# Performance work log

Hardware: AMD Instinct MI355X
Metric: run time of the kernel (lower is better)

The kernel has to match this reference:

```python
import jax, jax.numpy as jnp
import numpy as np

N = 8192   # nodes
F = 128    # input feature dim
U = 128    # units
EDGE_P = 0.002  # ~16 avg degree before symmetrization


def setup_inputs() -> dict:
    key = jax.random.key(0)
    k1, k2, k3 = jax.random.split(key, 3)
    a = (jax.random.uniform(k1, (N, N)) < EDGE_P).astype(jnp.float32)
    adj = jnp.maximum(a, a.T)  # symmetric binary adjacency, no self-loops
    x = jax.random.normal(k2, (N, F), dtype=jnp.float32)
    W = jax.random.normal(k3, (F, U), dtype=jnp.float32) * 0.05
    b = jnp.zeros((U,), dtype=jnp.float32)
    return {"x": x, "adj": adj, "W": W, "b": b}


def adj_norm(adj):
    # Kipf & Welling renormalization: A' = D^{-1/2} (A + I) D^{-1/2}
    a_hat = adj + jnp.eye(adj.shape[0], dtype=adj.dtype)
    d_inv_sqrt = jax.lax.rsqrt(jnp.sum(a_hat, axis=-1))
    return a_hat * d_inv_sqrt[:, None] * d_inv_sqrt[None, :]


def reference(x, adj, W, b):
    adj_n = adj_norm(adj)            # [N, N]
    h = adj_n @ x                    # [N, F] aggregation
    h = h @ W + b                    # [N, U] dense projection + bias
    return jax.nn.relu(h)
```

## Files before the change

### kernel.cpp

```cpp
#include <hip/hip_runtime.h>
#include <math.h>

#define N 8192
#define F 128
#define U 128
#define CAP 128
#define GEMM_BLOCKS 256
#define FCHUNK 32

typedef float f32x4 __attribute__((ext_vector_type(4)));
typedef unsigned short u16;
typedef unsigned int u32;

__device__ __forceinline__ int lane_off(unsigned long long m) {
    int c = __builtin_amdgcn_mbcnt_lo((unsigned)m, 0u);
    return __builtin_amdgcn_mbcnt_hi((unsigned)(m >> 32), c);
}

__device__ __forceinline__ u16 f2bf(float f) {
    u32 u = __float_as_uint(f);
    return (u16)((u + 0x7fffu + ((u >> 16) & 1u)) >> 16);
}
__device__ __forceinline__ float bflo(u32 v) { return __uint_as_float(v << 16); }
__device__ __forceinline__ float bfhi(u32 v) { return __uint_as_float(v & 0xffff0000u); }

__global__ __launch_bounds__(256) void k_scan_gemm(const float* __restrict__ adj,
                                                   const float* __restrict__ x,
                                                   const float* __restrict__ W,
                                                   float* __restrict__ dinv,
                                                   int* __restrict__ cnt,
                                                   u16* __restrict__ cols,
                                                   u16* __restrict__ y) {
    __shared__ float sW[FCHUNK * U];
    const int tid = threadIdx.x;

    if (blockIdx.x < GEMM_BLOCKS) {
        const int l  = tid & 31;
        const int p  = tid >> 5;
        const int n0 = blockIdx.x * 32 + p * 4;
        const float* xr = x + (size_t)n0 * F;

        float acc[4][4];
        #pragma unroll
        for (int i = 0; i < 4; ++i)
            #pragma unroll
            for (int u = 0; u < 4; ++u) acc[i][u] = 0.f;

        for (int chunk = 0; chunk < F / FCHUNK; ++chunk) {
            {
                const float4* Wp = (const float4*)(W + (size_t)chunk * FCHUNK * U);
                float4* sWp = (float4*)sW;
                #pragma unroll
                for (int k = 0; k < (FCHUNK * U / 4) / 256; ++k)
                    sWp[tid + k * 256] = Wp[tid + k * 256];
            }
            __syncthreads();

            const int fb = chunk * FCHUNK;
            #pragma unroll
            for (int f = 0; f < FCHUNK; f += 4) {
                f32x4 xa = *(const f32x4*)(xr + 0 * F + fb + f);
                f32x4 xb = *(const f32x4*)(xr + 1 * F + fb + f);
                f32x4 xc = *(const f32x4*)(xr + 2 * F + fb + f);
                f32x4 xd = *(const f32x4*)(xr + 3 * F + fb + f);
                #pragma unroll
                for (int k = 0; k < 4; ++k) {
                    const f32x4 w = *(const f32x4*)(sW + (f + k) * U + l * 4);
                    #pragma unroll
                    for (int u = 0; u < 4; ++u) {
                        acc[0][u] = fmaf(xa[k], w[u], acc[0][u]);
                        acc[1][u] = fmaf(xb[k], w[u], acc[1][u]);
                        acc[2][u] = fmaf(xc[k], w[u], acc[2][u]);
                        acc[3][u] = fmaf(xd[k], w[u], acc[3][u]);
                    }
                }
            }
            __syncthreads();
        }

        #pragma unroll
        for (int i = 0; i < 4; ++i) {
            ushort4 o;
            o.x = f2bf(acc[i][0]);
            o.y = f2bf(acc[i][1]);
            o.z = f2bf(acc[i][2]);
            o.w = f2bf(acc[i][3]);
            *(ushort4*)(y + (size_t)(n0 + i) * U + l * 4) = o;
        }
    } else {
        const int wid  = tid >> 6;
        const int lane = tid & 63;
        const int row  = (blockIdx.x - GEMM_BLOCKS) * 4 + wid;

        const f32x4* rp = (const f32x4*)(adj + (size_t)row * N);
        u16* crow = cols + (size_t)row * CAP;

        int base = 0;

        #pragma unroll 8
        for (int k = 0; k < N / 4 / 64; ++k) {
            const int fi = k * 64 + lane;
            const f32x4 v = __builtin_nontemporal_load(&rp[fi]);
            const int col = fi * 4;

            const unsigned long long m0 = __ballot(v[0] != 0.f);
            const unsigned long long m1 = __ballot(v[1] != 0.f);
            const unsigned long long m2 = __ballot(v[2] != 0.f);
            const unsigned long long m3 = __ballot(v[3] != 0.f);

            if (m0) { if (v[0] != 0.f) { int s = base + lane_off(m0); if (s < CAP) crow[s] = (u16)col;       } base += __popcll(m0); }
            if (m1) { if (v[1] != 0.f) { int s = base + lane_off(m1); if (s < CAP) crow[s] = (u16)(col + 1); } base += __popcll(m1); }
            if (m2) { if (v[2] != 0.f) { int s = base + lane_off(m2); if (s < CAP) crow[s] = (u16)(col + 2); } base += __popcll(m2); }
            if (m3) { if (v[3] != 0.f) { int s = base + lane_off(m3); if (s < CAP) crow[s] = (u16)(col + 3); } base += __popcll(m3); }
        }

        if (lane == 0) {
            dinv[row] = 1.0f / sqrtf((float)base + 1.0f);
            cnt[row]  = min(base, CAP);
        }
    }
}

__global__ __launch_bounds__(256, 4) void k_agg(const u16* __restrict__ y,
                                                const float* __restrict__ bias,
                                                const float* __restrict__ dinv,
                                                const int* __restrict__ cnt,
                                                const u16* __restrict__ cols,
                                                float* __restrict__ out) {
    const int wid  = threadIdx.x >> 6;
    const int lane = threadIdx.x & 63;
    const int node = blockIdx.x * 4 + wid;

    const int   c  = cnt[node];
    const float di = dinv[node];
    const u16* crow = cols + (size_t)node * CAP;

    const u32 self = *(const u32*)(y + (size_t)node * F + lane * 2);
    float acc0 = di * bflo(self);
    float acc1 = di * bfhi(self);

    for (int m0 = 0; m0 < c; m0 += 8) {
        const uint4 cw = *(const uint4*)(crow + m0);
        const u32 cwa[4] = {cw.x, cw.y, cw.z, cw.w};
        int   jj[8];
        float dj[8];
        #pragma unroll
        for (int k = 0; k < 8; ++k) {
            const int  jraw  = (int)((cwa[k >> 1] >> ((k & 1) * 16)) & 0xffffu);
            const bool valid = (m0 + k) < c;
            jj[k] = valid ? jraw : node;
            dj[k] = valid ? dinv[jj[k]] : 0.f;
        }
        #pragma unroll
        for (int k = 0; k < 8; ++k) {
            const u32 v = *(const u32*)(y + (size_t)jj[k] * F + lane * 2);
            acc0 = fmaf(dj[k], bflo(v), acc0);
            acc1 = fmaf(dj[k], bfhi(v), acc1);
        }
    }

    const float2 bb = *(const float2*)(bias + lane * 2);
    const float o0 = fmaxf(fmaf(di, acc0, bb.x), 0.f);
    const float o1 = fmaxf(fmaf(di, acc1, bb.y), 0.f);
    *(float2*)(out + (size_t)node * F + lane * 2) = make_float2(o0, o1);
}

extern "C" void kernel_launch(void* const* d_in, const int* in_sizes, int n_in,
                              void* d_out, int out_size, void* d_ws, size_t ws_size,
                              hipStream_t stream) {
    const float* x   = (const float*)d_in[0];
    const float* adj = (const float*)d_in[1];
    const float* W   = (const float*)d_in[2];
    const float* b   = (const float*)d_in[3];
    float* out = (float*)d_out;

    float* dinv = (float*)d_ws;
    int*   cnt  = (int*)((char*)d_ws + (size_t)N * 4);
    u16*   cols = (u16*)((char*)d_ws + (size_t)N * 8);
    u16*   yy   = (u16*)((char*)d_ws + (size_t)N * 8 + (size_t)N * CAP * 2);

    k_scan_gemm<<<GEMM_BLOCKS + N / 4, 256, 0, stream>>>(adj, x, W, dinv, cnt, cols, yy);
    k_agg      <<<N / 4,               256, 0, stream>>>(yy, b, dinv, cnt, cols, out);
}
```

Baseline: 67.95 us.

## Use atomic work-stealing over adjacency rows with batched loads in scan kernel

Replaces the static one-wave-per-row mapping of the adjacency scan with a persistent grid of 2048 blocks whose waves claim rows through a global atomic counter, zeroed by a memset before launch. GEMM blocks also join the scan once their projection is done. Each wave now issues eight 16-byte loads before running the ballots, to raise memory-level parallelism. Nontemporal loads are dropped. The aim is to balance work and keep more HBM reads in flight over the 256MB adjacency stream, at the cost of atomic contention, an extra memset call and higher register pressure.

```diff
diff --git a/kernel.cpp b/kernel.cpp
--- a/kernel.cpp
+++ b/kernel.cpp
@@ -7,6 +7,7 @@
 #define CAP 128
 #define GEMM_BLOCKS 256
 #define FCHUNK 32
+#define GRID_BLKS 2048
 
 typedef float f32x4 __attribute__((ext_vector_type(4)));
 typedef unsigned short u16;
@@ -24,13 +25,14 @@
 __device__ __forceinline__ float bflo(u32 v) { return __uint_as_float(v << 16); }
 __device__ __forceinline__ float bfhi(u32 v) { return __uint_as_float(v & 0xffff0000u); }
 
-__global__ __launch_bounds__(256) void k_scan_gemm(const float* __restrict__ adj,
-                                                   const float* __restrict__ x,
-                                                   const float* __restrict__ W,
-                                                   float* __restrict__ dinv,
-                                                   int* __restrict__ cnt,
-                                                   u16* __restrict__ cols,
-                                                   u16* __restrict__ y) {
+__global__ __launch_bounds__(256) void k_fused(const float* __restrict__ adj,
+                                               const float* __restrict__ x,
+                                               const float* __restrict__ W,
+                                               float* __restrict__ dinv,
+                                               int* __restrict__ cnt,
+                                               u16* __restrict__ cols,
+                                               u16* __restrict__ y,
+                                               int* __restrict__ ctr) {
     __shared__ float sW[FCHUNK * U];
     const int tid = threadIdx.x;
 
@@ -87,36 +89,45 @@
             o.w = f2bf(acc[i][3]);
             *(ushort4*)(y + (size_t)(n0 + i) * U + l * 4) = o;
         }
-    } else {
-        const int wid  = tid >> 6;
-        const int lane = tid & 63;
-        const int row  = (blockIdx.x - GEMM_BLOCKS) * 4 + wid;
+    }
 
-        const f32x4* rp = (const f32x4*)(adj + (size_t)row * N);
-        u16* crow = cols + (size_t)row * CAP;
+    const int lane = tid & 63;
+
+    for (;;) {
+        int r;
+        if (lane == 0) r = atomicAdd(ctr, 1);
+        r = __shfl(r, 0);
+        if (r >= N) break;
+
+        const f32x4* rp = (const f32x4*)(adj + (size_t)r * N);
+        u16* crow = cols + (size_t)r * CAP;
 
         int base = 0;
 
-        #pragma unroll 8
-        for (int k = 0; k < N / 4 / 64; ++k) {
-            const int fi = k * 64 + lane;
-            const f32x4 v = __builtin_nontemporal_load(&rp[fi]);
-            const int col = fi * 4;
+        for (int kb = 0; kb < 4; ++kb) {
+            f32x4 v[8];
+            #pragma unroll
+            for (int t = 0; t < 8; ++t)
+                v[t] = rp[(kb * 8 + t) * 64 + lane];
 
-            const unsigned long long m0 = __ballot(v[0] != 0.f);
-            const unsigned long long m1 = __ballot(v[1] != 0.f);
-            const unsigned long long m2 = __ballot(v[2] != 0.f);
-            const unsigned long long m3 = __ballot(v[3] != 0.f);
+            #pragma unroll
+            for (int t = 0; t < 8; ++t) {
+                const int col = ((kb * 8 + t) * 64 + lane) * 4;
+                const unsigned long long m0 = __ballot(v[t][0] != 0.f);
+                const unsigned long long m1 = __ballot(v[t][1] != 0.f);
+                const unsigned long long m2 = __ballot(v[t][2] != 0.f);
+                const unsigned long long m3 = __ballot(v[t][3] != 0.f);
 
-            if (m0) { if (v[0] != 0.f) { int s = base + lane_off(m0); if (s < CAP) crow[s] = (u16)col;       } base += __popcll(m0); }
-            if (m1) { if (v[1] != 0.f) { int s = base + lane_off(m1); if (s < CAP) crow[s] = (u16)(col + 1); } base += __popcll(m1); }
-            if (m2) { if (v[2] != 0.f) { int s = base + lane_off(m2); if (s < CAP) crow[s] = (u16)(col + 2); } base += __popcll(m2); }
-            if (m3) { if (v[3] != 0.f) { int s = base + lane_off(m3); if (s < CAP) crow[s] = (u16)(col + 3); } base += __popcll(m3); }
+                if (m0) { if (v[t][0] != 0.f) { int s = base + lane_off(m0); if (s < CAP) crow[s] = (u16)col;       } base += __popcll(m0); }
+                if (m1) { if (v[t][1] != 0.f) { int s = base + lane_off(m1); if (s < CAP) crow[s] = (u16)(col + 1); } base += __popcll(m1); }
+                if (m2) { if (v[t][2] != 0.f) { int s = base + lane_off(m2); if (s < CAP) crow[s] = (u16)(col + 2); } base += __popcll(m2); }
+                if (m3) { if (v[t][3] != 0.f) { int s = base + lane_off(m3); if (s < CAP) crow[s] = (u16)(col + 3); } base += __popcll(m3); }
+            }
         }
 
         if (lane == 0) {
-            dinv[row] = 1.0f / sqrtf((float)base + 1.0f);
-            cnt[row]  = min(base, CAP);
+            dinv[r] = 1.0f / sqrtf((float)base + 1.0f);
+            cnt[r]  = min(base, CAP);
         }
     }
 }
@@ -178,7 +189,9 @@
     int*   cnt  = (int*)((char*)d_ws + (size_t)N * 4);
     u16*   cols = (u16*)((char*)d_ws + (size_t)N * 8);
     u16*   yy   = (u16*)((char*)d_ws + (size_t)N * 8 + (size_t)N * CAP * 2);
+    int*   ctr  = (int*)((char*)d_ws + (size_t)N * 8 + (size_t)N * CAP * 2 + (size_t)N * U * 2);
 
-    k_scan_gemm<<<GEMM_BLOCKS + N / 4, 256, 0, stream>>>(adj, x, W, dinv, cnt, cols, yy);
-    k_agg      <<<N / 4,               256, 0, stream>>>(yy, b, dinv, cnt, cols, out);
+    hipMemsetAsync(ctr, 0, sizeof(int), stream);
+    k_fused<<<GRID_BLKS, 256, 0, stream>>>(adj, x, W, dinv, cnt, cols, yy, ctr);
+    k_agg  <<<N / 4,     256, 0, stream>>>(yy, b, dinv, cnt, cols, out);
 }
```

After: 225.8 us. 3.32x slower.
